# Kernel optimization log

Measured on AMD Instinct MI355X. Metric: run time of the kernel, lower is better.

Reference implementation:

```python
import jax, jax.numpy as jnp
import numpy as np

FEAT = 256
HID = FEAT // 2
N_KEYS = 2          # output_keys = ["energy_0", "energy_1"]
N_MOLS = 2000
ATOMS_PER_MOL = 100
N_ATOMS = N_MOLS * ATOMS_PER_MOL
LOG2 = 0.6931471805599453


def shifted_softplus(x):
    # NFF's shifted softplus: softplus(x) - log(2)
    return jax.nn.softplus(x) - LOG2


def setup_inputs() -> dict:
    key = jax.random.key(0)
    ks = jax.random.split(key, 6)
    s_i = jax.random.normal(ks[0], (N_ATOMS, FEAT), dtype=jnp.float32)
    xyz = jax.random.normal(ks[1], (N_ATOMS, 3), dtype=jnp.float32)
    num_atoms = jnp.full((N_MOLS,), ATOMS_PER_MOL, dtype=jnp.int64)
    # Per-key MLP params stacked over keys: Linear(F->H), act, Linear(H->1)
    W1 = jax.random.normal(ks[2], (N_KEYS, FEAT, HID), dtype=jnp.float32) / np.sqrt(FEAT)
    b1 = jnp.zeros((N_KEYS, HID), dtype=jnp.float32)
    W2 = jax.random.normal(ks[3], (N_KEYS, HID), dtype=jnp.float32) / np.sqrt(HID)
    b2 = jnp.zeros((N_KEYS,), dtype=jnp.float32)
    return {"s_i": s_i, "xyz": xyz, "num_atoms": num_atoms,
            "W1": W1, "b1": b1, "W2": W2, "b2": b2}


def reference(s_i, xyz, num_atoms, W1, b1, W2, b2):
    n_mols = num_atoms.shape[0]
    # segment id per atom, replacing the torch.split(...)+per-chunk sum loop
    seg = jnp.repeat(jnp.arange(n_mols), num_atoms,
                     total_repeat_length=s_i.shape[0])        # [N]
    # per-key MLP: [K,N,H] hidden, [K,N] scalar output per atom
    h = shifted_softplus(jnp.einsum('nf,kfh->knh', s_i, W1) + b1[:, None, :])
    val = jnp.einsum('knh,kh->kn', h, W2) + b2[:, None]       # [K, N]
    # fused segment-sum pooling -> per-molecule scalars
    pooled = jax.ops.segment_sum(val.T, seg, num_segments=n_mols)  # [M, K]
    return pooled.T                                            # [K, M]
```

## Files before the change

kernel.cpp:

```cpp
#include <hip/hip_runtime.h>

#define FEAT 256
#define HID 128
#define NKEYS 2

typedef __bf16 bf16x8 __attribute__((ext_vector_type(8)));
typedef float f32x16 __attribute__((ext_vector_type(16)));

union Frag {
    bf16x8 v;
    unsigned u[4];
    uint4 q;
};

__device__ __forceinline__ unsigned pack_bf16_2(float f0, float f1) {
    unsigned u0 = __float_as_uint(f0) + 0x8000u;
    unsigned u1 = __float_as_uint(f1) + 0x8000u;
    return __builtin_amdgcn_perm(u1, u0, 0x07060302u);
}

__device__ __forceinline__ float ssp(float x) {
    float sp = __logf(1.0f + __expf(x));
    sp = (x > 15.0f) ? x : sp;
    return sp - 0.69314718056f;
}

__device__ __forceinline__ int find_mol(const int* __restrict__ off, int n_mols, int g) {
    int lo = 0, hi = n_mols;
    while (hi - lo > 1) {
        int mid = (lo + hi) >> 1;
        if (off[mid] <= g) lo = mid; else hi = mid;
    }
    return lo;
}

__global__ void prep_kernel(const void* __restrict__ num_atoms_raw,
                            const float* __restrict__ W1,
                            int n_mols, int n_atoms,
                            int* __restrict__ off,
                            unsigned short* __restrict__ Bp,
                            float* __restrict__ out, int out_n) {
    if (blockIdx.x > 0) {
        int idx = (blockIdx.x - 1) * 256 + threadIdx.x;
        int c = idx >> 8;
        int k = idx & 255;
        int key = c >> 7, j = c & 127;
        float f = W1[(size_t)key * FEAT * HID + (size_t)k * HID + j];
        unsigned u = __float_as_uint(f);
        unsigned r = (u + 0x7FFFu + ((u >> 16) & 1u)) >> 16;
        Bp[(size_t)c * FEAT + k] = (unsigned short)r;
        return;
    }
    for (int i = threadIdx.x; i < out_n; i += 256) out[i] = 0.0f;

    __shared__ long long tsum[256];
    __shared__ int csum[257];
    __shared__ int mode_sh;
    int tid = threadIdx.x;
    const int* a32 = (const int*)num_atoms_raw;
    const long long* a64 = (const long long*)num_atoms_raw;
    int chunk = (n_mols + 255) >> 8;
    int lo = tid * chunk;
    if (lo > n_mols) lo = n_mols;
    int hi = lo + chunk;
    if (hi > n_mols) hi = n_mols;
    long long s = 0;
    for (int i = lo; i < hi; ++i) s += (long long)a32[i];
    tsum[tid] = s;
    __syncthreads();
    if (tid == 0) {
        long long t = 0;
        for (int i = 0; i < 256; ++i) t += tsum[i];
        mode_sh = (t == (long long)n_atoms) ? 0 : 1;
    }
    __syncthreads();
    int mode = mode_sh;
    if (mode) {
        s = 0;
        for (int i = lo; i < hi; ++i) s += a64[i];
        tsum[tid] = s;
    }
    csum[tid] = (int)tsum[tid];
    __syncthreads();
    if (tid == 0) {
        int run = 0;
        for (int i = 0; i < 256; ++i) { int v = csum[i]; csum[i] = run; run += v; }
    }
    __syncthreads();
    int run = csum[tid];
    for (int i = lo; i < hi; ++i) {
        off[i] = run;
        run += mode ? (int)a64[i] : a32[i];
    }
    if (hi >= n_mols) off[n_mols] = run;
}

__global__ __launch_bounds__(256, 2)
void gemm_fused(const float* __restrict__ A,
                const unsigned short* __restrict__ Bp,
                const float* __restrict__ b1,
                const float* __restrict__ W2,
                const float* __restrict__ b2,
                const int* __restrict__ off,
                float* __restrict__ out,
                int n_atoms, int n_mols) {
    __shared__ uint4 ldsA[64 * 8];
    __shared__ float part[4][64];
    __shared__ float molacc[NKEYS][4];

    const int tid  = threadIdx.x;
    const int lane = tid & 63;
    const int wn   = tid >> 6;
    const int l31  = lane & 31;
    const int half = lane >> 5;
    const int m0   = blockIdx.x * 64;

    const int srow = tid >> 2;
    const int sseg = tid & 3;
    int grow = m0 + srow;
    if (grow > n_atoms - 1) grow = n_atoms - 1;
    const float4* gsrc = (const float4*)(A + (size_t)grow * FEAT + sseg * 16);
    const int wu0 = srow * 8 + (((sseg * 2)    ) ^ (srow & 7));
    const int wu1 = srow * 8 + (((sseg * 2) + 1) ^ (srow & 7));

    const int c0 = wn * 64 + l31;
    const unsigned short* bb0 = Bp + (size_t)c0 * FEAT + half * 8;
    const unsigned short* bb1 = Bp + (size_t)(c0 + 32) * FEAT + half * 8;
    const int rbase0 = l31 * 8;
    const int rbase1 = (l31 + 32) * 8;
    const int rxor = l31 & 7;

    f32x16 acc00 = 0.0f, acc01 = 0.0f, acc10 = 0.0f, acc11 = 0.0f;

    #pragma unroll
    for (int c = 0; c < FEAT / 64; ++c) {
        const int kb = c * 64;
        Frag bf0[4], bf1[4];
        #pragma unroll
        for (int j = 0; j < 4; ++j) {
            bf0[j].q = *(const uint4*)(bb0 + kb + j * 16);
            bf1[j].q = *(const uint4*)(bb1 + kb + j * 16);
        }
        float4 f0 = gsrc[c * 16 + 0];
        float4 f1 = gsrc[c * 16 + 1];
        float4 f2 = gsrc[c * 16 + 2];
        float4 f3 = gsrc[c * 16 + 3];
        if (c > 0) __syncthreads();
        uint4 p0, p1;
        p0.x = pack_bf16_2(f0.x, f0.y);
        p0.y = pack_bf16_2(f0.z, f0.w);
        p0.z = pack_bf16_2(f1.x, f1.y);
        p0.w = pack_bf16_2(f1.z, f1.w);
        p1.x = pack_bf16_2(f2.x, f2.y);
        p1.y = pack_bf16_2(f2.z, f2.w);
        p1.z = pack_bf16_2(f3.x, f3.y);
        p1.w = pack_bf16_2(f3.z, f3.w);
        ldsA[wu0] = p0;
        ldsA[wu1] = p1;
        __syncthreads();

        #pragma unroll
        for (int j = 0; j < 4; ++j) {
            const int u = j * 2 + half;
            const int sw = u ^ rxor;
            Frag a0, a1;
            a0.q = ldsA[rbase0 + sw];
            a1.q = ldsA[rbase1 + sw];
            acc00 = __builtin_amdgcn_mfma_f32_32x32x16_bf16(a0.v, bf0[j].v, acc00, 0, 0, 0);
            acc01 = __builtin_amdgcn_mfma_f32_32x32x16_bf16(a0.v, bf1[j].v, acc01, 0, 0, 0);
            acc10 = __builtin_amdgcn_mfma_f32_32x32x16_bf16(a1.v, bf0[j].v, acc10, 0, 0, 0);
            acc11 = __builtin_amdgcn_mfma_f32_32x32x16_bf16(a1.v, bf1[j].v, acc11, 0, 0, 0);
        }
    }

    if (tid < NKEYS * 4) molacc[tid >> 2][tid & 3] = 0.0f;

    float b1c0 = b1[c0], b1c1 = b1[c0 + 32];
    float w2c0 = W2[c0], w2c1 = W2[c0 + 32];

    #pragma unroll
    for (int rt = 0; rt < 2; ++rt) {
        const f32x16& Ac0 = rt ? acc10 : acc00;
        const f32x16& Ac1 = rt ? acc11 : acc01;
        #pragma unroll
        for (int r = 0; r < 16; ++r) {
            float t = ssp(Ac0[r] + b1c0) * w2c0 + ssp(Ac1[r] + b1c1) * w2c1;
            t += __shfl_xor(t, 1);
            t += __shfl_xor(t, 2);
            t += __shfl_xor(t, 4);
            t += __shfl_xor(t, 8);
            t += __shfl_xor(t, 16);
            if (l31 == r) {
                int row = rt * 32 + (r & 3) + 8 * (r >> 2) + 4 * half;
                part[wn][row] = t;
            }
        }
    }
    __syncthreads();

    if (tid < NKEYS * 64) {
        int key = tid >> 6, r = tid & 63;
        int gm = m0 + r;
        if (gm < n_atoms) {
            float val = part[2 * key][r] + part[2 * key + 1][r] + b2[key];
            int mol  = find_mol(off, n_mols, gm);
            int mol0 = find_mol(off, n_mols, m0);
            int ml = mol - mol0;
            if (ml < 4) atomicAdd(&molacc[key][ml], val);
            else        atomicAdd(&out[(size_t)key * n_mols + mol], val);
        }
    }
    __syncthreads();

    if (tid < NKEYS * 4) {
        int key = tid >> 2, ml = tid & 3;
        int mol0 = find_mol(off, n_mols, m0);
        int mol = mol0 + ml;
        if (mol < n_mols) {
            float v = molacc[key][ml];
            if (v != 0.0f) atomicAdd(&out[(size_t)key * n_mols + mol], v);
        }
    }
}

extern "C" void kernel_launch(void* const* d_in, const int* in_sizes, int n_in,
                              void* d_out, int out_size, void* d_ws, size_t ws_size,
                              hipStream_t stream) {
    const float* s_i      = (const float*)d_in[0];
    const void*  num_atoms = d_in[2];
    const float* W1 = (const float*)d_in[3];
    const float* b1 = (const float*)d_in[4];
    const float* W2 = (const float*)d_in[5];
    const float* b2 = (const float*)d_in[6];
    int n_atoms = in_sizes[0] / FEAT;
    int n_mols  = in_sizes[2];
    float* out = (float*)d_out;

    int* off = (int*)d_ws;
    size_t off_bytes = (((size_t)(n_mols + 1) * 4) + 255) & ~(size_t)255;
    unsigned short* Bp = (unsigned short*)((char*)d_ws + off_bytes);

    int pack_blocks = (NKEYS * HID * FEAT) / 256;
    prep_kernel<<<1 + pack_blocks, 256, 0, stream>>>(num_atoms, W1, n_mols, n_atoms,
                                                     off, Bp, out, out_size);

    int gblocks = (n_atoms + 63) / 64;
    gemm_fused<<<gblocks, 256, 0, stream>>>(s_i, Bp, b1, W2, b2, off, out, n_atoms, n_mols);
}
```

Baseline: 347.8 us.

## Double-buffer A tile in LDS, prefetch B fragments, cache row molecule ids

The GEMM main loop now double-buffers the bf16 A tile in shared memory. The next chunk's global loads are issued before the MFMAs of the current chunk, and the B fragments are prefetched one step ahead, which should overlap memory latency with compute and halve the barriers. The molecule lookup (binary search) is done once per row at kernel start and stored in shared memory instead of being repeated in the epilogue. Launch bounds rise to 4 blocks per CU, which adds register pressure. The prep kernel's serial reductions are replaced with parallel tree reduction and Hillis-Steele scan.

```diff
diff --git a/kernel.cpp b/kernel.cpp
--- a/kernel.cpp
+++ b/kernel.cpp
@@ -54,8 +54,7 @@
     for (int i = threadIdx.x; i < out_n; i += 256) out[i] = 0.0f;
 
     __shared__ long long tsum[256];
-    __shared__ int csum[257];
-    __shared__ int mode_sh;
+    __shared__ int csum[256];
     int tid = threadIdx.x;
     const int* a32 = (const int*)num_atoms_raw;
     const long long* a64 = (const long long*)num_atoms_raw;
@@ -64,30 +63,33 @@
     if (lo > n_mols) lo = n_mols;
     int hi = lo + chunk;
     if (hi > n_mols) hi = n_mols;
-    long long s = 0;
-    for (int i = lo; i < hi; ++i) s += (long long)a32[i];
-    tsum[tid] = s;
-    __syncthreads();
-    if (tid == 0) {
-        long long t = 0;
-        for (int i = 0; i < 256; ++i) t += tsum[i];
-        mode_sh = (t == (long long)n_atoms) ? 0 : 1;
-    }
-    __syncthreads();
-    int mode = mode_sh;
+
+    long long s32 = 0;
+    for (int i = lo; i < hi; ++i) s32 += (long long)a32[i];
+    tsum[tid] = s32;
+    __syncthreads();
+    #pragma unroll
+    for (int d = 128; d > 0; d >>= 1) {
+        if (tid < d) tsum[tid] += tsum[tid + d];
+        __syncthreads();
+    }
+    int mode = (tsum[0] == (long long)n_atoms) ? 0 : 1;
+    long long s = s32;
     if (mode) {
         s = 0;
         for (int i = lo; i < hi; ++i) s += a64[i];
-        tsum[tid] = s;
-    }
-    csum[tid] = (int)tsum[tid];
-    __syncthreads();
-    if (tid == 0) {
-        int run = 0;
-        for (int i = 0; i < 256; ++i) { int v = csum[i]; csum[i] = run; run += v; }
-    }
-    __syncthreads();
-    int run = csum[tid];
+    }
+    int v = (int)s;
+    csum[tid] = v;
+    __syncthreads();
+    #pragma unroll
+    for (int d = 1; d < 256; d <<= 1) {
+        int t = (tid >= d) ? csum[tid - d] : 0;
+        __syncthreads();
+        csum[tid] += t;
+        __syncthreads();
+    }
+    int run = csum[tid] - v;
     for (int i = lo; i < hi; ++i) {
         off[i] = run;
         run += mode ? (int)a64[i] : a32[i];
@@ -95,7 +97,7 @@
     if (hi >= n_mols) off[n_mols] = run;
 }
 
-__global__ __launch_bounds__(256, 2)
+__global__ __launch_bounds__(256, 4)
 void gemm_fused(const float* __restrict__ A,
                 const unsigned short* __restrict__ Bp,
                 const float* __restrict__ b1,
@@ -104,9 +106,10 @@
                 const int* __restrict__ off,
                 float* __restrict__ out,
                 int n_atoms, int n_mols) {
-    __shared__ uint4 ldsA[64 * 8];
+    __shared__ uint4 ldsA[2][64 * 8];
     __shared__ float part[4][64];
     __shared__ float molacc[NKEYS][4];
+    __shared__ int rowmol[64];
 
     const int tid  = threadIdx.x;
     const int lane = tid & 63;
@@ -130,22 +133,23 @@
     const int rbase1 = (l31 + 32) * 8;
     const int rxor = l31 & 7;
 
+    float4 f0 = gsrc[0];
+    float4 f1 = gsrc[1];
+    float4 f2 = gsrc[2];
+    float4 f3 = gsrc[3];
+
+    if (tid < 64) {
+        int gm = m0 + tid;
+        if (gm > n_atoms - 1) gm = n_atoms - 1;
+        rowmol[tid] = find_mol(off, n_mols, gm);
+    }
+    if (tid < NKEYS * 4) molacc[tid >> 2][tid & 3] = 0.0f;
+    const float b1c0 = b1[c0], b1c1 = b1[c0 + 32];
+    const float w2c0 = W2[c0], w2c1 = W2[c0 + 32];
+
     f32x16 acc00 = 0.0f, acc01 = 0.0f, acc10 = 0.0f, acc11 = 0.0f;
 
-    #pragma unroll
-    for (int c = 0; c < FEAT / 64; ++c) {
-        const int kb = c * 64;
-        Frag bf0[4], bf1[4];
-        #pragma unroll
-        for (int j = 0; j < 4; ++j) {
-            bf0[j].q = *(const uint4*)(bb0 + kb + j * 16);
-            bf1[j].q = *(const uint4*)(bb1 + kb + j * 16);
-        }
-        float4 f0 = gsrc[c * 16 + 0];
-        float4 f1 = gsrc[c * 16 + 1];
-        float4 f2 = gsrc[c * 16 + 2];
-        float4 f3 = gsrc[c * 16 + 3];
-        if (c > 0) __syncthreads();
+    {
         uint4 p0, p1;
         p0.x = pack_bf16_2(f0.x, f0.y);
         p0.y = pack_bf16_2(f0.z, f0.w);
@@ -155,28 +159,56 @@
         p1.y = pack_bf16_2(f2.z, f2.w);
         p1.z = pack_bf16_2(f3.x, f3.y);
         p1.w = pack_bf16_2(f3.z, f3.w);
-        ldsA[wu0] = p0;
-        ldsA[wu1] = p1;
-        __syncthreads();
-
+        ldsA[0][wu0] = p0;
+        ldsA[0][wu1] = p1;
+    }
+    __syncthreads();
+
+    #pragma unroll
+    for (int c = 0; c < FEAT / 64; ++c) {
+        const int kb = c * 64;
+        if (c < 3) {
+            f0 = gsrc[(c + 1) * 16 + 0];
+            f1 = gsrc[(c + 1) * 16 + 1];
+            f2 = gsrc[(c + 1) * 16 + 2];
+            f3 = gsrc[(c + 1) * 16 + 3];
+        }
+        const uint4* lbuf = ldsA[c & 1];
+        Frag b0c, b1c, b0n, b1n;
+        b0c.q = *(const uint4*)(bb0 + kb);
+        b1c.q = *(const uint4*)(bb1 + kb);
         #pragma unroll
         for (int j = 0; j < 4; ++j) {
-            const int u = j * 2 + half;
-            const int sw = u ^ rxor;
+            if (j < 3) {
+                b0n.q = *(const uint4*)(bb0 + kb + (j + 1) * 16);
+                b1n.q = *(const uint4*)(bb1 + kb + (j + 1) * 16);
+            }
+            const int sw = (j * 2 + half) ^ rxor;
             Frag a0, a1;
-            a0.q = ldsA[rbase0 + sw];
-            a1.q = ldsA[rbase1 + sw];
-            acc00 = __builtin_amdgcn_mfma_f32_32x32x16_bf16(a0.v, bf0[j].v, acc00, 0, 0, 0);
-            acc01 = __builtin_amdgcn_mfma_f32_32x32x16_bf16(a0.v, bf1[j].v, acc01, 0, 0, 0);
-            acc10 = __builtin_amdgcn_mfma_f32_32x32x16_bf16(a1.v, bf0[j].v, acc10, 0, 0, 0);
-            acc11 = __builtin_amdgcn_mfma_f32_32x32x16_bf16(a1.v, bf1[j].v, acc11, 0, 0, 0);
-        }
-    }
-
-    if (tid < NKEYS * 4) molacc[tid >> 2][tid & 3] = 0.0f;
-
-    float b1c0 = b1[c0], b1c1 = b1[c0 + 32];
-    float w2c0 = W2[c0], w2c1 = W2[c0 + 32];
+            a0.q = lbuf[rbase0 + sw];
+            a1.q = lbuf[rbase1 + sw];
+            acc00 = __builtin_amdgcn_mfma_f32_32x32x16_bf16(a0.v, b0c.v, acc00, 0, 0, 0);
+            acc01 = __builtin_amdgcn_mfma_f32_32x32x16_bf16(a0.v, b1c.v, acc01, 0, 0, 0);
+            acc10 = __builtin_amdgcn_mfma_f32_32x32x16_bf16(a1.v, b0c.v, acc10, 0, 0, 0);
+            acc11 = __builtin_amdgcn_mfma_f32_32x32x16_bf16(a1.v, b1c.v, acc11, 0, 0, 0);
+            b0c = b0n;
+            b1c = b1n;
+        }
+        if (c < 3) {
+            uint4 p0, p1;
+            p0.x = pack_bf16_2(f0.x, f0.y);
+            p0.y = pack_bf16_2(f0.z, f0.w);
+            p0.z = pack_bf16_2(f1.x, f1.y);
+            p0.w = pack_bf16_2(f1.z, f1.w);
+            p1.x = pack_bf16_2(f2.x, f2.y);
+            p1.y = pack_bf16_2(f2.z, f2.w);
+            p1.z = pack_bf16_2(f3.x, f3.y);
+            p1.w = pack_bf16_2(f3.z, f3.w);
+            ldsA[(c + 1) & 1][wu0] = p0;
+            ldsA[(c + 1) & 1][wu1] = p1;
+            __syncthreads();
+        }
+    }
 
     #pragma unroll
     for (int rt = 0; rt < 2; ++rt) {
@@ -203,9 +235,8 @@
         int gm = m0 + r;
         if (gm < n_atoms) {
             float val = part[2 * key][r] + part[2 * key + 1][r] + b2[key];
-            int mol  = find_mol(off, n_mols, gm);
-            int mol0 = find_mol(off, n_mols, m0);
-            int ml = mol - mol0;
+            int mol = rowmol[r];
+            int ml  = mol - rowmol[0];
             if (ml < 4) atomicAdd(&molacc[key][ml], val);
             else        atomicAdd(&out[(size_t)key * n_mols + mol], val);
         }
@@ -214,8 +245,7 @@
 
     if (tid < NKEYS * 4) {
         int key = tid >> 2, ml = tid & 3;
-        int mol0 = find_mol(off, n_mols, m0);
-        int mol = mol0 + ml;
+        int mol = rowmol[0] + ml;
         if (mol < n_mols) {
             float v = molacc[key][ml];
             if (v != 0.0f) atomicAdd(&out[(size_t)key * n_mols + mol], v);
```

Measured after the change: 340.6 us. -2.1%, faster.

## Load full A tile via global_load_lds, convert to bf16 at fragment read, stage offsets in LDS

Applied to the files above, without the earlier changes.

Replaces the per-chunk register load, pack and LDS-store loop with direct global-to-LDS async loads of the whole 64x256 fp32 tile up front, followed by a single barrier. The bf16 conversion moves to fragment read time, and the per-chunk barriers are gone. The molecule offset table is also staged into LDS for the binary searches, and the prep kernel's serial reductions become tree reductions and scans. This raises LDS use to 64KB per block, which may lower occupancy, and it repeats the conversion work for each B tile.

```diff
diff --git a/kernel.cpp b/kernel.cpp
--- a/kernel.cpp
+++ b/kernel.cpp
@@ -25,13 +25,20 @@
     return sp - 0.69314718056f;
 }
 
-__device__ __forceinline__ int find_mol(const int* __restrict__ off, int n_mols, int g) {
+__device__ __forceinline__ int find_mol(const int* off, int n_mols, int g) {
     int lo = 0, hi = n_mols;
     while (hi - lo > 1) {
         int mid = (lo + hi) >> 1;
         if (off[mid] <= g) lo = mid; else hi = mid;
     }
     return lo;
+}
+
+__device__ __forceinline__ void gload_lds16(const float* g, void* l) {
+    __builtin_amdgcn_global_load_lds(
+        (const __attribute__((address_space(1))) unsigned int*)g,
+        (__attribute__((address_space(3))) unsigned int*)l,
+        16, 0, 0);
 }
 
 __global__ void prep_kernel(const void* __restrict__ num_atoms_raw,
@@ -54,8 +61,7 @@
     for (int i = threadIdx.x; i < out_n; i += 256) out[i] = 0.0f;
 
     __shared__ long long tsum[256];
-    __shared__ int csum[257];
-    __shared__ int mode_sh;
+    __shared__ int csum[256];
     int tid = threadIdx.x;
     const int* a32 = (const int*)num_atoms_raw;
     const long long* a64 = (const long long*)num_atoms_raw;
@@ -64,30 +70,33 @@
     if (lo > n_mols) lo = n_mols;
     int hi = lo + chunk;
     if (hi > n_mols) hi = n_mols;
-    long long s = 0;
-    for (int i = lo; i < hi; ++i) s += (long long)a32[i];
-    tsum[tid] = s;
-    __syncthreads();
-    if (tid == 0) {
-        long long t = 0;
-        for (int i = 0; i < 256; ++i) t += tsum[i];
-        mode_sh = (t == (long long)n_atoms) ? 0 : 1;
-    }
-    __syncthreads();
-    int mode = mode_sh;
+
+    long long s32 = 0;
+    for (int i = lo; i < hi; ++i) s32 += (long long)a32[i];
+    tsum[tid] = s32;
+    __syncthreads();
+    #pragma unroll
+    for (int d = 128; d > 0; d >>= 1) {
+        if (tid < d) tsum[tid] += tsum[tid + d];
+        __syncthreads();
+    }
+    int mode = (tsum[0] == (long long)n_atoms) ? 0 : 1;
+    long long s = s32;
     if (mode) {
         s = 0;
         for (int i = lo; i < hi; ++i) s += a64[i];
-        tsum[tid] = s;
-    }
-    csum[tid] = (int)tsum[tid];
-    __syncthreads();
-    if (tid == 0) {
-        int run = 0;
-        for (int i = 0; i < 256; ++i) { int v = csum[i]; csum[i] = run; run += v; }
-    }
-    __syncthreads();
-    int run = csum[tid];
+    }
+    int v = (int)s;
+    csum[tid] = v;
+    __syncthreads();
+    #pragma unroll
+    for (int d = 1; d < 256; d <<= 1) {
+        int t = (tid >= d) ? csum[tid - d] : 0;
+        __syncthreads();
+        csum[tid] += t;
+        __syncthreads();
+    }
+    int run = csum[tid] - v;
     for (int i = lo; i < hi; ++i) {
         off[i] = run;
         run += mode ? (int)a64[i] : a32[i];
@@ -104,36 +113,55 @@
                 const int* __restrict__ off,
                 float* __restrict__ out,
                 int n_atoms, int n_mols) {
-    __shared__ uint4 ldsA[64 * 8];
-    __shared__ float part[4][64];
-    __shared__ float molacc[NKEYS][4];
+    __shared__ uint4 ldsA[4096];
+    int*   offlds = (int*)ldsA;
+    float (*part)[64] = (float(*)[64])((char*)ldsA + 8192);
+    float (*molacc)[4] = (float(*)[4])((char*)ldsA + 9216);
+    int*   mol0sh = (int*)((char*)ldsA + 9248);
 
     const int tid  = threadIdx.x;
     const int lane = tid & 63;
-    const int wn   = tid >> 6;
+    const int wid  = tid >> 6;
     const int l31  = lane & 31;
     const int half = lane >> 5;
     const int m0   = blockIdx.x * 64;
 
-    const int srow = tid >> 2;
-    const int sseg = tid & 3;
-    int grow = m0 + srow;
-    if (grow > n_atoms - 1) grow = n_atoms - 1;
-    const float4* gsrc = (const float4*)(A + (size_t)grow * FEAT + sseg * 16);
-    const int wu0 = srow * 8 + (((sseg * 2)    ) ^ (srow & 7));
-    const int wu1 = srow * 8 + (((sseg * 2) + 1) ^ (srow & 7));
-
-    const int c0 = wn * 64 + l31;
+    const bool lds_off_ok = (n_mols + 1) <= 2048;
+    int4 ov0, ov1;
+    if (lds_off_ok) {
+        const int4* o4 = (const int4*)off;
+        ov0 = o4[tid * 2];
+        ov1 = o4[tid * 2 + 1];
+    }
+
+    #pragma unroll
+    for (int i = 0; i < 4; ++i) {
+        const int p   = i * 256 + wid * 64 + lane;
+        const int row = p >> 4;
+        const int u   = (p & 15) ^ (row & 15);
+        int gr = m0 + row;
+        if (gr > n_atoms - 1) gr = n_atoms - 1;
+        const float* g = A + (size_t)gr * FEAT + u * 4;
+        #pragma unroll
+        for (int c = 0; c < 4; ++c) {
+            gload_lds16(g + c * 64, (void*)&ldsA[c * 1024 + i * 256 + wid * 64]);
+        }
+    }
+
+    const int c0 = wid * 64 + l31;
     const unsigned short* bb0 = Bp + (size_t)c0 * FEAT + half * 8;
     const unsigned short* bb1 = Bp + (size_t)(c0 + 32) * FEAT + half * 8;
-    const int rbase0 = l31 * 8;
-    const int rbase1 = (l31 + 32) * 8;
-    const int rxor = l31 & 7;
+    const int s = l31 & 15;
+    const float b1c0 = b1[c0], b1c1 = b1[c0 + 32];
+    const float w2c0 = W2[c0], w2c1 = W2[c0 + 32];
+
+    __syncthreads();
 
     f32x16 acc00 = 0.0f, acc01 = 0.0f, acc10 = 0.0f, acc11 = 0.0f;
 
     #pragma unroll
-    for (int c = 0; c < FEAT / 64; ++c) {
+    for (int c = 0; c < 4; ++c) {
+        const uint4* lbuf = ldsA + c * 1024;
         const int kb = c * 64;
         Frag bf0[4], bf1[4];
         #pragma unroll
@@ -141,31 +169,29 @@
             bf0[j].q = *(const uint4*)(bb0 + kb + j * 16);
             bf1[j].q = *(const uint4*)(bb1 + kb + j * 16);
         }
-        float4 f0 = gsrc[c * 16 + 0];
-        float4 f1 = gsrc[c * 16 + 1];
-        float4 f2 = gsrc[c * 16 + 2];
-        float4 f3 = gsrc[c * 16 + 3];
-        if (c > 0) __syncthreads();
-        uint4 p0, p1;
-        p0.x = pack_bf16_2(f0.x, f0.y);
-        p0.y = pack_bf16_2(f0.z, f0.w);
-        p0.z = pack_bf16_2(f1.x, f1.y);
-        p0.w = pack_bf16_2(f1.z, f1.w);
-        p1.x = pack_bf16_2(f2.x, f2.y);
-        p1.y = pack_bf16_2(f2.z, f2.w);
-        p1.z = pack_bf16_2(f3.x, f3.y);
-        p1.w = pack_bf16_2(f3.z, f3.w);
-        ldsA[wu0] = p0;
-        ldsA[wu1] = p1;
-        __syncthreads();
-
         #pragma unroll
         for (int j = 0; j < 4; ++j) {
-            const int u = j * 2 + half;
-            const int sw = u ^ rxor;
+            const int u0 = j * 4 + half * 2;
+            const int q0 = u0 ^ s;
+            const int base0 = l31 * 16;
+            const int base1 = (l31 + 32) * 16;
+            uint4 lo0 = lbuf[base0 + q0];
+            uint4 hi0 = lbuf[base0 + (q0 ^ 1)];
+            uint4 lo1 = lbuf[base1 + q0];
+            uint4 hi1 = lbuf[base1 + (q0 ^ 1)];
+            const float4 fl0 = *(const float4*)&lo0;
+            const float4 fh0 = *(const float4*)&hi0;
+            const float4 fl1 = *(const float4*)&lo1;
+            const float4 fh1 = *(const float4*)&hi1;
             Frag a0, a1;
-            a0.q = ldsA[rbase0 + sw];
-            a1.q = ldsA[rbase1 + sw];
+            a0.u[0] = pack_bf16_2(fl0.x, fl0.y);
+            a0.u[1] = pack_bf16_2(fl0.z, fl0.w);
+            a0.u[2] = pack_bf16_2(fh0.x, fh0.y);
+            a0.u[3] = pack_bf16_2(fh0.z, fh0.w);
+            a1.u[0] = pack_bf16_2(fl1.x, fl1.y);
+            a1.u[1] = pack_bf16_2(fl1.z, fl1.w);
+            a1.u[2] = pack_bf16_2(fh1.x, fh1.y);
+            a1.u[3] = pack_bf16_2(fh1.z, fh1.w);
             acc00 = __builtin_amdgcn_mfma_f32_32x32x16_bf16(a0.v, bf0[j].v, acc00, 0, 0, 0);
             acc01 = __builtin_amdgcn_mfma_f32_32x32x16_bf16(a0.v, bf1[j].v, acc01, 0, 0, 0);
             acc10 = __builtin_amdgcn_mfma_f32_32x32x16_bf16(a1.v, bf0[j].v, acc10, 0, 0, 0);
@@ -173,10 +199,13 @@
         }
     }
 
+    __syncthreads();
+
+    if (lds_off_ok) {
+        ((int4*)offlds)[tid * 2]     = ov0;
+        ((int4*)offlds)[tid * 2 + 1] = ov1;
+    }
     if (tid < NKEYS * 4) molacc[tid >> 2][tid & 3] = 0.0f;
-
-    float b1c0 = b1[c0], b1c1 = b1[c0 + 32];
-    float w2c0 = W2[c0], w2c1 = W2[c0 + 32];
 
     #pragma unroll
     for (int rt = 0; rt < 2; ++rt) {
@@ -192,7 +221,7 @@
             t += __shfl_xor(t, 16);
             if (l31 == r) {
                 int row = rt * 32 + (r & 3) + 8 * (r >> 2) + 4 * half;
-                part[wn][row] = t;
+                part[wid][row] = t;
             }
         }
     }
@@ -201,10 +230,12 @@
     if (tid < NKEYS * 64) {
         int key = tid >> 6, r = tid & 63;
         int gm = m0 + r;
+        const int* o = lds_off_ok ? offlds : off;
+        int mol0 = find_mol(o, n_mols, m0);
+        if (tid == 0) *mol0sh = mol0;
         if (gm < n_atoms) {
+            int mol = find_mol(o, n_mols, gm);
             float val = part[2 * key][r] + part[2 * key + 1][r] + b2[key];
-            int mol  = find_mol(off, n_mols, gm);
-            int mol0 = find_mol(off, n_mols, m0);
             int ml = mol - mol0;
             if (ml < 4) atomicAdd(&molacc[key][ml], val);
             else        atomicAdd(&out[(size_t)key * n_mols + mol], val);
@@ -214,8 +245,7 @@
 
     if (tid < NKEYS * 4) {
         int key = tid >> 2, ml = tid & 3;
-        int mol0 = find_mol(off, n_mols, m0);
-        int mol = mol0 + ml;
+        int mol = *mol0sh + ml;
         if (mol < n_mols) {
             float v = molacc[key][ml];
             if (v != 0.0f) atomicAdd(&out[(size_t)key * n_mols + mol], v);
```

Measured after the change: 389.0 us. +11.8%, slower.
